# Optimization experiments

Hardware: AMD Instinct MI355X
Metric: run time of the kernel (lower is better)

The kernel has to match this reference:

```python
import jax, jax.numpy as jnp
import numpy as np

GAMMA = 1.0
BIG = 1e10  # finite stand-in for +inf (keeps logsumexp/vjp NaN-free; exp(-BIG/gamma)==0)


def _softmin3(a, b, c, gamma):
    # -gamma * logsumexp(-x/gamma) over the three candidates
    s = jnp.stack([a, b, c], axis=0) * (-1.0 / gamma)
    return -gamma * jax.scipy.special.logsumexp(s, axis=0)


def _softdtw(D, gamma):
    """Soft-DTW cost via anti-diagonal wavefront scan.
    D: (B, N, M) distance matrix. Returns (B,) soft-DTW cost R[N, M].
    Diagonal d holds cells (i, j) with i + j == d; stored as length-(N+1)
    vectors indexed by i, invalid cells = BIG.
    """
    B, N, M = D.shape
    ii = jnp.arange(N)  # ii = i - 1 for cells i = 1..N on a diagonal

    # diagonal d=0: only R[0,0]=0; diagonal d=1: all padded-inf cells
    r_d0 = jnp.full((B, N + 1), BIG, D.dtype).at[:, 0].set(0.0)
    r_d1 = jnp.full((B, N + 1), BIG, D.dtype)

    def step(carry, d):
        rp2, rp1 = carry  # diagonals d-2 and d-1, each (B, N+1)
        jj = d - 2 - ii  # jj = j - 1 = d - i - 1 for each cell on diagonal d
        valid = (jj >= 0) & (jj < M)  # j in 1..M (i in 1..N by construction)
        d_vals = D[:, ii, jnp.clip(jj, 0, M - 1)]  # (B, N): D[:, i-1, j-1]
        # cell i uses R[i-1,j-1]=rp2[i-1], R[i-1,j]=rp1[i-1], R[i,j-1]=rp1[i]
        sm = _softmin3(rp2[:, :-1], rp1[:, :-1], rp1[:, 1:], gamma)  # (B, N)
        new_inner = jnp.where(valid[None, :], d_vals + sm, BIG)
        row0 = jnp.full((B, 1), BIG, D.dtype)  # i = 0 row is always inf for d >= 2
        new_diag = jnp.concatenate([row0, new_inner], axis=1)  # (B, N+1)
        return (rp1, new_diag), None

    (_, r_last), _ = jax.lax.scan(step, (r_d0, r_d1), jnp.arange(2, N + M + 1))
    return r_last[:, N]  # R[N, M]


def setup_inputs() -> dict:
    key = jax.random.key(0)
    D = jax.random.uniform(key, (64, 1024, 1024), dtype=jnp.float32)
    return {"D": D}


def reference(D):
    return _softdtw(D, GAMMA)
```

## Files before the change

### kernel.cpp

```cpp
#include <hip/hip_runtime.h>


#define LOG2E 1.4426950408889634f
#define LN2  0.6931471805599453f

constexpr int N = 1024;
constexpr int TPB = 64;
constexpr int KC = 8;
constexpr int RQ = 4;
constexpr int NQ = N / RQ;
constexpr int NPAN = 2;
constexpr int PC = N / NPAN;
constexpr int ITER = 320;
constexpr unsigned long long POISON = 0xFFFFFFFFFFFFFFFFull;

__device__ __forceinline__ float fexp2(float x){float r;asm("v_exp_f32 %0, %1":"=v"(r):"v"(x));return r;}
__device__ __forceinline__ float flog2(float x){float r;asm("v_log_f32 %0, %1":"=v"(r):"v"(x));return r;}
__device__ __forceinline__ int   ffrexpe(float x){int r;asm("v_frexp_exp_i32_f32 %0, %1":"=v"(r):"v"(x));return r;}
__device__ __forceinline__ float fldexp(float x, int e){float r;asm("v_ldexp_f32 %0, %1, %2":"=v"(r):"v"(x),"v"(e));return r;}

__device__ __forceinline__ unsigned long long packv(float a, float b){
    return ((unsigned long long)__float_as_uint(b) << 32) | __float_as_uint(a);
}
__device__ __forceinline__ unsigned long long ldrelax(const unsigned long long* p){
    return __hip_atomic_load(p, __ATOMIC_RELAXED, __HIP_MEMORY_SCOPE_AGENT);
}

__global__ __launch_bounds__(TPB, 1)
void softdtw_kernel(const float* __restrict__ D, float* __restrict__ out,
                    unsigned long long* __restrict__ pay){
    const int blk = blockIdx.x;
    const int b = blk & 63;
    const int q = blk >> 6;
    const int t = threadIdx.x;
    const float* __restrict__ bp = D + (size_t)b * N * N + q * PC + t * KC;

    const bool isProd = (t == TPB - 1) && (q == 0);
    const bool isCons = (t == 0) && (q == 1);
    const size_t base = (size_t)b * NQ * 2;

    float pW[KC] = {0,0,0,0,0,0,0,0};
    int   S = 0;
    float luW = (t == 0 && q == 0) ? 1.0f : 0.0f;
    float exW[RQ] = {0,0,0,0};
    int   exS = 0;
    float nW[RQ] = {0,0,0,0};
    int   nS = 0;

    unsigned long long rg[8][2];
#pragma unroll
    for (int i = 0; i < 8; ++i) { rg[i][0] = POISON; rg[i][1] = POISON; }
    if (isCons) {
#pragma unroll
        for (int i = 0; i < 8; ++i) {
            rg[i][0] = ldrelax(&pay[base + (size_t)i * 2 + 0]);
            rg[i][1] = ldrelax(&pay[base + (size_t)i * 2 + 1]);
        }
    }

    float4 ld[2][RQ][2];
#pragma unroll
    for (int x = 0; x < 2; ++x) {
        int pc = min(max(x - t, 0), NQ - 1);
        const float* a = bp + (size_t)(pc * RQ) * N;
#pragma unroll
        for (int r = 0; r < RQ; ++r) {
            ld[x][r][0] = *(const float4*)(a + (size_t)r * N);
            ld[x][r][1] = *(const float4*)(a + (size_t)r * N + 4);
        }
    }
    __builtin_amdgcn_sched_barrier(0);

    for (int jb = 0; jb < ITER; jb += 8) {
#pragma unroll
        for (int u = 0; u < 8; ++u) {
            const int p = jb + u - t;
            const bool active = (unsigned)p < (unsigned)NQ;
            const int slot = u & 1;

            float cv0 = 0, cv1 = 0, cv2 = 0, cv3 = 0;
            if (isCons && active) {
                unsigned long long w0 = rg[u][0];
                unsigned long long w1 = rg[u][1];
                while (w0 == POISON) w0 = ldrelax(&pay[base + (size_t)p * 2 + 0]);
                while (w1 == POISON) w1 = ldrelax(&pay[base + (size_t)p * 2 + 1]);
                cv0 = __uint_as_float((unsigned)(w0 & 0xFFFFFFFFu));
                cv1 = __uint_as_float((unsigned)(w0 >> 32));
                cv2 = __uint_as_float((unsigned)(w1 & 0xFFFFFFFFu));
                cv3 = __uint_as_float((unsigned)(w1 >> 32));
            }

            const int iS = nS;
            if (p == 0) {
                if (isCons) S = (int)(0.0f - cv0);
                else if (t == 0 && q == 0) S = 0;
                else S = iS;
            }

            float eW[RQ];
            {
                const int dS = iS - S;
                eW[0] = fldexp(nW[0], dS); eW[1] = fldexp(nW[1], dS);
                eW[2] = fldexp(nW[2], dS); eW[3] = fldexp(nW[3], dS);
            }
            if (t == 0 && q == 0) { eW[0] = eW[1] = eW[2] = eW[3] = 0.0f; }
            if (isCons) {
                const float Sf = (float)S;
                eW[0] = fexp2(0.0f - cv0 - Sf);
                eW[1] = fexp2(0.0f - cv1 - Sf);
                eW[2] = fexp2(0.0f - cv2 - Sf);
                eW[3] = fexp2(0.0f - cv3 - Sf);
            }

            float a0 = pW[0], a1 = pW[1], a2 = pW[2], a3 = pW[3];
            float a4 = pW[4], a5 = pW[5], a6 = pW[6], a7 = pW[7];
            float dg = luW;
            float eR[RQ];
#pragma unroll
            for (int r = 0; r < RQ; ++r) {
                const float4 d0 = ld[slot][r][0];
                const float4 d1 = ld[slot][r][1];
                float f0 = fexp2(-LOG2E * d0.x), f1 = fexp2(-LOG2E * d0.y);
                float f2 = fexp2(-LOG2E * d0.z), f3 = fexp2(-LOG2E * d0.w);
                float f4 = fexp2(-LOG2E * d1.x), f5 = fexp2(-LOG2E * d1.y);
                float f6 = fexp2(-LOG2E * d1.z), f7 = fexp2(-LOG2E * d1.w);
                float s01 = a0 + a1, s12 = a1 + a2, s23 = a2 + a3, s34 = a3 + a4;
                float s45 = a4 + a5, s56 = a5 + a6, s67 = a6 + a7;
                float t0 = dg + eW[r];
                float W0 = f0 * (a0 + t0);
                float W1 = f1 * (s01 + W0);
                float W2 = f2 * (s12 + W1);
                float W3 = f3 * (s23 + W2);
                float W4 = f4 * (s34 + W3);
                float W5 = f5 * (s45 + W4);
                float W6 = f6 * (s56 + W5);
                float W7 = f7 * (s67 + W6);
                eR[r] = W7;
                dg = eW[r];
                a0 = W0; a1 = W1; a2 = W2; a3 = W3;
                a4 = W4; a5 = W5; a6 = W6; a7 = W7;
            }

            const int e = ffrexpe(a7);
            const float sc = fldexp(1.0f, -e);

            if (active) {
                pW[0] = a0 * sc; pW[1] = a1 * sc; pW[2] = a2 * sc; pW[3] = a3 * sc;
                pW[4] = a4 * sc; pW[5] = a5 * sc; pW[6] = a6 * sc; pW[7] = a7 * sc;
                luW = dg * sc;
                exW[0] = eR[0] * sc; exW[1] = eR[1] * sc;
                exW[2] = eR[2] * sc; exW[3] = eR[3] * sc;
                S += e; exS = S;
            }

            if (isProd && active) {
                const float Sf = (float)S;
                float v0 = 0.0f - (flog2(exW[0]) + Sf);
                float v1 = 0.0f - (flog2(exW[1]) + Sf);
                float v2 = 0.0f - (flog2(exW[2]) + Sf);
                float v3 = 0.0f - (flog2(exW[3]) + Sf);
                __hip_atomic_store(&pay[base + (size_t)p * 2 + 0], packv(v0, v1), __ATOMIC_RELAXED, __HIP_MEMORY_SCOPE_AGENT);
                __hip_atomic_store(&pay[base + (size_t)p * 2 + 1], packv(v2, v3), __ATOMIC_RELAXED, __HIP_MEMORY_SCOPE_AGENT);
            }

            {
                int pc = min(max(p + 2, 0), NQ - 1);
                const float* a = bp + (size_t)(pc * RQ) * N;
#pragma unroll
                for (int r = 0; r < RQ; ++r) {
                    ld[slot][r][0] = *(const float4*)(a + (size_t)r * N);
                    ld[slot][r][1] = *(const float4*)(a + (size_t)r * N + 4);
                }
            }
            __builtin_amdgcn_sched_barrier(0);

            if (isCons && (p + 8) < NQ) {
                rg[u][0] = ldrelax(&pay[base + (size_t)(p + 8) * 2 + 0]);
                rg[u][1] = ldrelax(&pay[base + (size_t)(p + 8) * 2 + 1]);
            }

            nW[0] = __shfl_up(exW[0], 1);
            nW[1] = __shfl_up(exW[1], 1);
            nW[2] = __shfl_up(exW[2], 1);
            nW[3] = __shfl_up(exW[3], 1);
            nS    = __shfl_up(exS, 1);
        }
    }

    if (q == NPAN - 1 && t == TPB - 1)
        out[b] = -(flog2(pW[KC - 1]) + (float)S) * LN2;
}

extern "C" void kernel_launch(void* const* d_in, const int* in_sizes, int n_in,
                              void* d_out, int out_size, void* d_ws, size_t ws_size,
                              hipStream_t stream) {
    const float* D = (const float*)d_in[0];
    float* out = (float*)d_out;
    const int B = in_sizes[0] / (N * N);

    unsigned long long* pay = (unsigned long long*)d_ws;
    const size_t payBytes = (size_t)B * NQ * 2 * sizeof(unsigned long long);

    hipMemsetAsync(d_ws, 0xFF, payBytes, stream);

    softdtw_kernel<<<B * NPAN, TPB, 0, stream>>>(D, out, pay);
}
```

Measured before the change: 254.6 us.

## Add producer wavefront that stages D tiles in LDS for compute wave

```diff
diff --git a/kernel.cpp b/kernel.cpp
--- a/kernel.cpp
+++ b/kernel.cpp
@@ -5,7 +5,7 @@
 #define LN2  0.6931471805599453f
 
 constexpr int N = 1024;
-constexpr int TPB = 64;
+constexpr int TPB = 128;
 constexpr int KC = 8;
 constexpr int RQ = 4;
 constexpr int NQ = N / RQ;
@@ -18,7 +18,9 @@
 __device__ __forceinline__ float flog2(float x){float r;asm("v_log_f32 %0, %1":"=v"(r):"v"(x));return r;}
 __device__ __forceinline__ int   ffrexpe(float x){int r;asm("v_frexp_exp_i32_f32 %0, %1":"=v"(r):"v"(x));return r;}
 __device__ __forceinline__ float fldexp(float x, int e){float r;asm("v_ldexp_f32 %0, %1, %2":"=v"(r):"v"(x),"v"(e));return r;}
-
+__device__ __forceinline__ void gload4(float4& d, const float* p){
+    asm volatile("global_load_dwordx4 %0, %1, off" : "=v"(d) : "v"(p));
+}
 __device__ __forceinline__ unsigned long long packv(float a, float b){
     return ((unsigned long long)__float_as_uint(b) << 32) | __float_as_uint(a);
 }
@@ -33,15 +35,69 @@
     const int b = blk & 63;
     const int q = blk >> 6;
     const int t = threadIdx.x;
-    const float* __restrict__ bp = D + (size_t)b * N * N + q * PC + t * KC;
-
-    const bool isProd = (t == TPB - 1) && (q == 0);
-    const bool isCons = (t == 0) && (q == 1);
+    const int lg = t & 63;
+    const int w = t >> 6;
+    const float* __restrict__ bp = D + (size_t)b * N * N + q * PC + lg * KC;
     const size_t base = (size_t)b * NQ * 2;
+
+    __shared__ float4 tile[4][RQ][2][64];
+    __shared__ int lseqv;
+    __shared__ int cdonev;
+    if (t == 0) { lseqv = -1; cdonev = -1; }
+    __syncthreads();
+
+    if (w == 1) {
+        float4 A[RQ][2], B[RQ][2];
+        const float* a0;
+        {
+            int pc = min(max(0 - lg, 0), NQ - 1);
+            a0 = bp + (size_t)(pc * RQ) * N;
+#pragma unroll
+            for (int r = 0; r < RQ; ++r) { gload4(A[r][0], a0 + (size_t)r * N); gload4(A[r][1], a0 + (size_t)r * N + 4); }
+            pc = min(max(1 - lg, 0), NQ - 1);
+            a0 = bp + (size_t)(pc * RQ) * N;
+#pragma unroll
+            for (int r = 0; r < RQ; ++r) { gload4(B[r][0], a0 + (size_t)r * N); gload4(B[r][1], a0 + (size_t)r * N + 4); }
+        }
+        for (int jb = 0; jb < ITER; jb += 2) {
+            {
+                const int jt = jb;
+                if (jt >= 4) { while (*(volatile int*)&cdonev < jt - 4) {} }
+                asm volatile("s_waitcnt vmcnt(8)" ::: "memory");
+                __builtin_amdgcn_sched_barrier(0);
+#pragma unroll
+                for (int r = 0; r < RQ; ++r) { tile[jt & 3][r][0][lg] = A[r][0]; tile[jt & 3][r][1][lg] = A[r][1]; }
+                asm volatile("s_waitcnt lgkmcnt(0)" ::: "memory");
+                *(volatile int*)&lseqv = jt;
+                int pc = min(max(jt + 2 - lg, 0), NQ - 1);
+                const float* a = bp + (size_t)(pc * RQ) * N;
+#pragma unroll
+                for (int r = 0; r < RQ; ++r) { gload4(A[r][0], a + (size_t)r * N); gload4(A[r][1], a + (size_t)r * N + 4); }
+            }
+            {
+                const int jt = jb + 1;
+                if (jt >= 4) { while (*(volatile int*)&cdonev < jt - 4) {} }
+                asm volatile("s_waitcnt vmcnt(8)" ::: "memory");
+                __builtin_amdgcn_sched_barrier(0);
+#pragma unroll
+                for (int r = 0; r < RQ; ++r) { tile[jt & 3][r][0][lg] = B[r][0]; tile[jt & 3][r][1][lg] = B[r][1]; }
+                asm volatile("s_waitcnt lgkmcnt(0)" ::: "memory");
+                *(volatile int*)&lseqv = jt;
+                int pc = min(max(jt + 2 - lg, 0), NQ - 1);
+                const float* a = bp + (size_t)(pc * RQ) * N;
+#pragma unroll
+                for (int r = 0; r < RQ; ++r) { gload4(B[r][0], a + (size_t)r * N); gload4(B[r][1], a + (size_t)r * N + 4); }
+            }
+        }
+        return;
+    }
+
+    const bool isProd = (lg == 63) && (q == 0);
+    const bool isCons = (lg == 0) && (q == 1);
 
     float pW[KC] = {0,0,0,0,0,0,0,0};
     int   S = 0;
-    float luW = (t == 0 && q == 0) ? 1.0f : 0.0f;
+    float luW = (lg == 0 && q == 0) ? 1.0f : 0.0f;
     float exW[RQ] = {0,0,0,0};
     int   exS = 0;
     float nW[RQ] = {0,0,0,0};
@@ -58,25 +114,12 @@
         }
     }
 
-    float4 ld[2][RQ][2];
-#pragma unroll
-    for (int x = 0; x < 2; ++x) {
-        int pc = min(max(x - t, 0), NQ - 1);
-        const float* a = bp + (size_t)(pc * RQ) * N;
-#pragma unroll
-        for (int r = 0; r < RQ; ++r) {
-            ld[x][r][0] = *(const float4*)(a + (size_t)r * N);
-            ld[x][r][1] = *(const float4*)(a + (size_t)r * N + 4);
-        }
-    }
-    __builtin_amdgcn_sched_barrier(0);
-
     for (int jb = 0; jb < ITER; jb += 8) {
 #pragma unroll
         for (int u = 0; u < 8; ++u) {
-            const int p = jb + u - t;
+            const int j = jb + u;
+            const int p = j - lg;
             const bool active = (unsigned)p < (unsigned)NQ;
-            const int slot = u & 1;
 
             float cv0 = 0, cv1 = 0, cv2 = 0, cv3 = 0;
             if (isCons && active) {
@@ -93,7 +136,7 @@
             const int iS = nS;
             if (p == 0) {
                 if (isCons) S = (int)(0.0f - cv0);
-                else if (t == 0 && q == 0) S = 0;
+                else if (lg == 0 && q == 0) S = 0;
                 else S = iS;
             }
 
@@ -103,7 +146,7 @@
                 eW[0] = fldexp(nW[0], dS); eW[1] = fldexp(nW[1], dS);
                 eW[2] = fldexp(nW[2], dS); eW[3] = fldexp(nW[3], dS);
             }
-            if (t == 0 && q == 0) { eW[0] = eW[1] = eW[2] = eW[3] = 0.0f; }
+            if (lg == 0 && q == 0) { eW[0] = eW[1] = eW[2] = eW[3] = 0.0f; }
             if (isCons) {
                 const float Sf = (float)S;
                 eW[0] = fexp2(0.0f - cv0 - Sf);
@@ -112,14 +155,20 @@
                 eW[3] = fexp2(0.0f - cv3 - Sf);
             }
 
+            while (*(volatile int*)&lseqv < j) {}
+            asm volatile("" ::: "memory");
+            float4 d0r[RQ], d1r[RQ];
+#pragma unroll
+            for (int r = 0; r < RQ; ++r) { d0r[r] = tile[j & 3][r][0][lg]; d1r[r] = tile[j & 3][r][1][lg]; }
+
             float a0 = pW[0], a1 = pW[1], a2 = pW[2], a3 = pW[3];
             float a4 = pW[4], a5 = pW[5], a6 = pW[6], a7 = pW[7];
             float dg = luW;
             float eR[RQ];
 #pragma unroll
             for (int r = 0; r < RQ; ++r) {
-                const float4 d0 = ld[slot][r][0];
-                const float4 d1 = ld[slot][r][1];
+                const float4 d0 = d0r[r];
+                const float4 d1 = d1r[r];
                 float f0 = fexp2(-LOG2E * d0.x), f1 = fexp2(-LOG2E * d0.y);
                 float f2 = fexp2(-LOG2E * d0.z), f3 = fexp2(-LOG2E * d0.w);
                 float f4 = fexp2(-LOG2E * d1.x), f5 = fexp2(-LOG2E * d1.y);
@@ -163,16 +212,8 @@
                 __hip_atomic_store(&pay[base + (size_t)p * 2 + 1], packv(v2, v3), __ATOMIC_RELAXED, __HIP_MEMORY_SCOPE_AGENT);
             }
 
-            {
-                int pc = min(max(p + 2, 0), NQ - 1);
-                const float* a = bp + (size_t)(pc * RQ) * N;
-#pragma unroll
-                for (int r = 0; r < RQ; ++r) {
-                    ld[slot][r][0] = *(const float4*)(a + (size_t)r * N);
-                    ld[slot][r][1] = *(const float4*)(a + (size_t)r * N + 4);
-                }
-            }
-            __builtin_amdgcn_sched_barrier(0);
+            asm volatile("" ::: "memory");
+            if (lg == 0) *(volatile int*)&cdonev = j;
 
             if (isCons && (p + 8) < NQ) {
                 rg[u][0] = ldrelax(&pay[base + (size_t)(p + 8) * 2 + 0]);
@@ -187,7 +228,7 @@
         }
     }
 
-    if (q == NPAN - 1 && t == TPB - 1)
+    if (q == NPAN - 1 && lg == 63)
         out[b] = -(flog2(pW[KC - 1]) + (float)S) * LN2;
 }
 
```

New measurement: 341.0 us. +34.0%, slower.

## Precompute exp(-D) into a per-thread contiguous strip layout in a prepass

Applied to the files above, without the earlier changes.

```diff
diff --git a/kernel.cpp b/kernel.cpp
--- a/kernel.cpp
+++ b/kernel.cpp
@@ -14,11 +14,15 @@
 constexpr int ITER = 320;
 constexpr unsigned long long POISON = 0xFFFFFFFFFFFFFFFFull;
 
+constexpr int STRIP_FLOATS = NQ * 32;
+constexpr int JOB_FLOATS   = 64 * STRIP_FLOATS;
+constexpr size_t MBOX_BYTES = (size_t)64 * NQ * 2 * sizeof(unsigned long long);
+constexpr size_t DP_BYTES   = (size_t)128 * JOB_FLOATS * sizeof(float);
+
 __device__ __forceinline__ float fexp2(float x){float r;asm("v_exp_f32 %0, %1":"=v"(r):"v"(x));return r;}
 __device__ __forceinline__ float flog2(float x){float r;asm("v_log_f32 %0, %1":"=v"(r):"v"(x));return r;}
 __device__ __forceinline__ int   ffrexpe(float x){int r;asm("v_frexp_exp_i32_f32 %0, %1":"=v"(r):"v"(x));return r;}
 __device__ __forceinline__ float fldexp(float x, int e){float r;asm("v_ldexp_f32 %0, %1, %2":"=v"(r):"v"(x),"v"(e));return r;}
-
 __device__ __forceinline__ unsigned long long packv(float a, float b){
     return ((unsigned long long)__float_as_uint(b) << 32) | __float_as_uint(a);
 }
@@ -26,14 +30,68 @@
     return __hip_atomic_load(p, __ATOMIC_RELAXED, __HIP_MEMORY_SCOPE_AGENT);
 }
 
+__global__ __launch_bounds__(256)
+void prepass_kernel(const float* __restrict__ D, float* __restrict__ Dp){
+    const int blk = blockIdx.x;
+    const int rb  = blk & 7;
+    const int g   = (blk >> 3) & 15;
+    const int job = blk >> 7;
+    const int b = job & 63, q = job >> 6;
+    const int tid = threadIdx.x;
+
+    __shared__ float lds[128 * 33];
+
+    {
+        const int row  = tid >> 1;
+        const int half = tid & 1;
+        const float* src = D + (size_t)b * N * N + (size_t)(rb * 128 + row) * N
+                         + q * PC + g * 32 + half * 16;
+        float4 v0 = *(const float4*)(src + 0);
+        float4 v1 = *(const float4*)(src + 4);
+        float4 v2 = *(const float4*)(src + 8);
+        float4 v3 = *(const float4*)(src + 12);
+        float* l = &lds[row * 33 + half * 16];
+        l[0]  = fexp2(-LOG2E * v0.x); l[1]  = fexp2(-LOG2E * v0.y);
+        l[2]  = fexp2(-LOG2E * v0.z); l[3]  = fexp2(-LOG2E * v0.w);
+        l[4]  = fexp2(-LOG2E * v1.x); l[5]  = fexp2(-LOG2E * v1.y);
+        l[6]  = fexp2(-LOG2E * v1.z); l[7]  = fexp2(-LOG2E * v1.w);
+        l[8]  = fexp2(-LOG2E * v2.x); l[9]  = fexp2(-LOG2E * v2.y);
+        l[10] = fexp2(-LOG2E * v2.z); l[11] = fexp2(-LOG2E * v2.w);
+        l[12] = fexp2(-LOG2E * v3.x); l[13] = fexp2(-LOG2E * v3.y);
+        l[14] = fexp2(-LOG2E * v3.z); l[15] = fexp2(-LOG2E * v3.w);
+    }
+    __syncthreads();
+
+    {
+        const int u    = tid >> 1;
+        const int half = tid & 1;
+        const int s    = u >> 5;
+        const int pl   = u & 31;
+        float o[16];
+#pragma unroll
+        for (int r2 = 0; r2 < 2; ++r2)
+#pragma unroll
+            for (int k = 0; k < 8; ++k)
+                o[r2 * 8 + k] = lds[(4 * pl + 2 * half + r2) * 33 + s * 8 + k];
+        float* dst = Dp + (size_t)job * JOB_FLOATS
+                   + (size_t)(g * 4 + s) * STRIP_FLOATS
+                   + (size_t)(rb * 32 + pl) * 32 + half * 16;
+        *(float4*)(dst + 0)  = make_float4(o[0], o[1], o[2], o[3]);
+        *(float4*)(dst + 4)  = make_float4(o[4], o[5], o[6], o[7]);
+        *(float4*)(dst + 8)  = make_float4(o[8], o[9], o[10], o[11]);
+        *(float4*)(dst + 12) = make_float4(o[12], o[13], o[14], o[15]);
+    }
+}
+
 __global__ __launch_bounds__(TPB, 1)
-void softdtw_kernel(const float* __restrict__ D, float* __restrict__ out,
+void softdtw_kernel(const float* __restrict__ Dp, float* __restrict__ out,
                     unsigned long long* __restrict__ pay){
     const int blk = blockIdx.x;
     const int b = blk & 63;
     const int q = blk >> 6;
     const int t = threadIdx.x;
-    const float* __restrict__ bp = D + (size_t)b * N * N + q * PC + t * KC;
+    const float* __restrict__ sp = Dp + (size_t)(q * 64 + b) * JOB_FLOATS
+                                 + (size_t)t * STRIP_FLOATS;
 
     const bool isProd = (t == TPB - 1) && (q == 0);
     const bool isCons = (t == 0) && (q == 1);
@@ -58,16 +116,13 @@
         }
     }
 
-    float4 ld[2][RQ][2];
+    float4 ld[2][8];
 #pragma unroll
     for (int x = 0; x < 2; ++x) {
         int pc = min(max(x - t, 0), NQ - 1);
-        const float* a = bp + (size_t)(pc * RQ) * N;
-#pragma unroll
-        for (int r = 0; r < RQ; ++r) {
-            ld[x][r][0] = *(const float4*)(a + (size_t)r * N);
-            ld[x][r][1] = *(const float4*)(a + (size_t)r * N + 4);
-        }
+        const float* a = sp + (size_t)pc * 32;
+#pragma unroll
+        for (int h = 0; h < 8; ++h) ld[x][h] = *(const float4*)(a + 4 * h);
     }
     __builtin_amdgcn_sched_barrier(0);
 
@@ -118,23 +173,19 @@
             float eR[RQ];
 #pragma unroll
             for (int r = 0; r < RQ; ++r) {
-                const float4 d0 = ld[slot][r][0];
-                const float4 d1 = ld[slot][r][1];
-                float f0 = fexp2(-LOG2E * d0.x), f1 = fexp2(-LOG2E * d0.y);
-                float f2 = fexp2(-LOG2E * d0.z), f3 = fexp2(-LOG2E * d0.w);
-                float f4 = fexp2(-LOG2E * d1.x), f5 = fexp2(-LOG2E * d1.y);
-                float f6 = fexp2(-LOG2E * d1.z), f7 = fexp2(-LOG2E * d1.w);
+                const float4 fa = ld[slot][r * 2 + 0];
+                const float4 fb = ld[slot][r * 2 + 1];
                 float s01 = a0 + a1, s12 = a1 + a2, s23 = a2 + a3, s34 = a3 + a4;
                 float s45 = a4 + a5, s56 = a5 + a6, s67 = a6 + a7;
                 float t0 = dg + eW[r];
-                float W0 = f0 * (a0 + t0);
-                float W1 = f1 * (s01 + W0);
-                float W2 = f2 * (s12 + W1);
-                float W3 = f3 * (s23 + W2);
-                float W4 = f4 * (s34 + W3);
-                float W5 = f5 * (s45 + W4);
-                float W6 = f6 * (s56 + W5);
-                float W7 = f7 * (s67 + W6);
+                float W0 = fa.x * (a0 + t0);
+                float W1 = fa.y * (s01 + W0);
+                float W2 = fa.z * (s12 + W1);
+                float W3 = fa.w * (s23 + W2);
+                float W4 = fb.x * (s34 + W3);
+                float W5 = fb.y * (s45 + W4);
+                float W6 = fb.z * (s56 + W5);
+                float W7 = fb.w * (s67 + W6);
                 eR[r] = W7;
                 dg = eW[r];
                 a0 = W0; a1 = W1; a2 = W2; a3 = W3;
@@ -165,12 +216,9 @@
 
             {
                 int pc = min(max(p + 2, 0), NQ - 1);
-                const float* a = bp + (size_t)(pc * RQ) * N;
-#pragma unroll
-                for (int r = 0; r < RQ; ++r) {
-                    ld[slot][r][0] = *(const float4*)(a + (size_t)r * N);
-                    ld[slot][r][1] = *(const float4*)(a + (size_t)r * N + 4);
-                }
+                const float* a = sp + (size_t)pc * 32;
+#pragma unroll
+                for (int h = 0; h < 8; ++h) ld[slot][h] = *(const float4*)(a + 4 * h);
             }
             __builtin_amdgcn_sched_barrier(0);
 
@@ -191,6 +239,120 @@
         out[b] = -(flog2(pW[KC - 1]) + (float)S) * LN2;
 }
 
+__global__ __launch_bounds__(TPB, 1)
+void softdtw_fb(const float* __restrict__ D, float* __restrict__ out,
+                unsigned long long* __restrict__ pay){
+    const int blk = blockIdx.x;
+    const int b = blk & 63, q = blk >> 6;
+    const int t = threadIdx.x;
+    const float* __restrict__ bp = D + (size_t)b * N * N + q * PC + t * KC;
+    const bool isProd = (t == TPB - 1) && (q == 0);
+    const bool isCons = (t == 0) && (q == 1);
+    const size_t base = (size_t)b * NQ * 2;
+    float pW[KC] = {0,0,0,0,0,0,0,0};
+    int S = 0; float luW = (t == 0 && q == 0) ? 1.0f : 0.0f;
+    float exW[RQ] = {0,0,0,0}; int exS = 0;
+    float nW[RQ] = {0,0,0,0}; int nS = 0;
+    unsigned long long rg[8][2];
+#pragma unroll
+    for (int i = 0; i < 8; ++i) { rg[i][0] = POISON; rg[i][1] = POISON; }
+    if (isCons) {
+#pragma unroll
+        for (int i = 0; i < 8; ++i) {
+            rg[i][0] = ldrelax(&pay[base + (size_t)i * 2 + 0]);
+            rg[i][1] = ldrelax(&pay[base + (size_t)i * 2 + 1]);
+        }
+    }
+    float4 ld[2][RQ][2];
+#pragma unroll
+    for (int x = 0; x < 2; ++x) {
+        int pc = min(max(x - t, 0), NQ - 1);
+        const float* a = bp + (size_t)(pc * RQ) * N;
+#pragma unroll
+        for (int r = 0; r < RQ; ++r) { ld[x][r][0] = *(const float4*)(a + (size_t)r * N); ld[x][r][1] = *(const float4*)(a + (size_t)r * N + 4); }
+    }
+    __builtin_amdgcn_sched_barrier(0);
+    for (int jb = 0; jb < ITER; jb += 8) {
+#pragma unroll
+        for (int u = 0; u < 8; ++u) {
+            const int p = jb + u - t;
+            const bool active = (unsigned)p < (unsigned)NQ;
+            const int slot = u & 1;
+            float cv0 = 0, cv1 = 0, cv2 = 0, cv3 = 0;
+            if (isCons && active) {
+                unsigned long long w0 = rg[u][0], w1 = rg[u][1];
+                while (w0 == POISON) w0 = ldrelax(&pay[base + (size_t)p * 2 + 0]);
+                while (w1 == POISON) w1 = ldrelax(&pay[base + (size_t)p * 2 + 1]);
+                cv0 = __uint_as_float((unsigned)(w0 & 0xFFFFFFFFu));
+                cv1 = __uint_as_float((unsigned)(w0 >> 32));
+                cv2 = __uint_as_float((unsigned)(w1 & 0xFFFFFFFFu));
+                cv3 = __uint_as_float((unsigned)(w1 >> 32));
+            }
+            const int iS = nS;
+            if (p == 0) { if (isCons) S = (int)(0.0f - cv0); else if (t == 0 && q == 0) S = 0; else S = iS; }
+            float eW[RQ];
+            { const int dS = iS - S;
+              eW[0] = fldexp(nW[0], dS); eW[1] = fldexp(nW[1], dS);
+              eW[2] = fldexp(nW[2], dS); eW[3] = fldexp(nW[3], dS); }
+            if (t == 0 && q == 0) { eW[0] = eW[1] = eW[2] = eW[3] = 0.0f; }
+            if (isCons) {
+                const float Sf = (float)S;
+                eW[0] = fexp2(0.0f - cv0 - Sf); eW[1] = fexp2(0.0f - cv1 - Sf);
+                eW[2] = fexp2(0.0f - cv2 - Sf); eW[3] = fexp2(0.0f - cv3 - Sf);
+            }
+            float a0 = pW[0], a1 = pW[1], a2 = pW[2], a3 = pW[3];
+            float a4 = pW[4], a5 = pW[5], a6 = pW[6], a7 = pW[7];
+            float dg = luW; float eR[RQ];
+#pragma unroll
+            for (int r = 0; r < RQ; ++r) {
+                const float4 d0 = ld[slot][r][0]; const float4 d1 = ld[slot][r][1];
+                float f0 = fexp2(-LOG2E * d0.x), f1 = fexp2(-LOG2E * d0.y);
+                float f2 = fexp2(-LOG2E * d0.z), f3 = fexp2(-LOG2E * d0.w);
+                float f4 = fexp2(-LOG2E * d1.x), f5 = fexp2(-LOG2E * d1.y);
+                float f6 = fexp2(-LOG2E * d1.z), f7 = fexp2(-LOG2E * d1.w);
+                float s01 = a0 + a1, s12 = a1 + a2, s23 = a2 + a3, s34 = a3 + a4;
+                float s45 = a4 + a5, s56 = a5 + a6, s67 = a6 + a7;
+                float t0 = dg + eW[r];
+                float W0 = f0 * (a0 + t0); float W1 = f1 * (s01 + W0);
+                float W2 = f2 * (s12 + W1); float W3 = f3 * (s23 + W2);
+                float W4 = f4 * (s34 + W3); float W5 = f5 * (s45 + W4);
+                float W6 = f6 * (s56 + W5); float W7 = f7 * (s67 + W6);
+                eR[r] = W7; dg = eW[r];
+                a0 = W0; a1 = W1; a2 = W2; a3 = W3; a4 = W4; a5 = W5; a6 = W6; a7 = W7;
+            }
+            const int e = ffrexpe(a7); const float sc = fldexp(1.0f, -e);
+            if (active) {
+                pW[0] = a0 * sc; pW[1] = a1 * sc; pW[2] = a2 * sc; pW[3] = a3 * sc;
+                pW[4] = a4 * sc; pW[5] = a5 * sc; pW[6] = a6 * sc; pW[7] = a7 * sc;
+                luW = dg * sc;
+                exW[0] = eR[0] * sc; exW[1] = eR[1] * sc; exW[2] = eR[2] * sc; exW[3] = eR[3] * sc;
+                S += e; exS = S;
+            }
+            if (isProd && active) {
+                const float Sf = (float)S;
+                float v0 = 0.0f - (flog2(exW[0]) + Sf), v1 = 0.0f - (flog2(exW[1]) + Sf);
+                float v2 = 0.0f - (flog2(exW[2]) + Sf), v3 = 0.0f - (flog2(exW[3]) + Sf);
+                __hip_atomic_store(&pay[base + (size_t)p * 2 + 0], packv(v0, v1), __ATOMIC_RELAXED, __HIP_MEMORY_SCOPE_AGENT);
+                __hip_atomic_store(&pay[base + (size_t)p * 2 + 1], packv(v2, v3), __ATOMIC_RELAXED, __HIP_MEMORY_SCOPE_AGENT);
+            }
+            { int pc = min(max(p + 2, 0), NQ - 1);
+              const float* a = bp + (size_t)(pc * RQ) * N;
+#pragma unroll
+              for (int r = 0; r < RQ; ++r) { ld[slot][r][0] = *(const float4*)(a + (size_t)r * N); ld[slot][r][1] = *(const float4*)(a + (size_t)r * N + 4); } }
+            __builtin_amdgcn_sched_barrier(0);
+            if (isCons && (p + 8) < NQ) {
+                rg[u][0] = ldrelax(&pay[base + (size_t)(p + 8) * 2 + 0]);
+                rg[u][1] = ldrelax(&pay[base + (size_t)(p + 8) * 2 + 1]);
+            }
+            nW[0] = __shfl_up(exW[0], 1); nW[1] = __shfl_up(exW[1], 1);
+            nW[2] = __shfl_up(exW[2], 1); nW[3] = __shfl_up(exW[3], 1);
+            nS = __shfl_up(exS, 1);
+        }
+    }
+    if (q == NPAN - 1 && t == TPB - 1)
+        out[b] = -(flog2(pW[KC - 1]) + (float)S) * LN2;
+}
+
 extern "C" void kernel_launch(void* const* d_in, const int* in_sizes, int n_in,
                               void* d_out, int out_size, void* d_ws, size_t ws_size,
                               hipStream_t stream) {
@@ -199,9 +361,13 @@
     const int B = in_sizes[0] / (N * N);
 
     unsigned long long* pay = (unsigned long long*)d_ws;
-    const size_t payBytes = (size_t)B * NQ * 2 * sizeof(unsigned long long);
-
-    hipMemsetAsync(d_ws, 0xFF, payBytes, stream);
-
-    softdtw_kernel<<<B * NPAN, TPB, 0, stream>>>(D, out, pay);
-}
+    hipMemsetAsync(d_ws, 0xFF, MBOX_BYTES, stream);
+
+    if (ws_size >= MBOX_BYTES + DP_BYTES && B == 64) {
+        float* Dp = (float*)((char*)d_ws + MBOX_BYTES);
+        prepass_kernel<<<128 * 16 * 8, 256, 0, stream>>>(D, Dp);
+        softdtw_kernel<<<B * NPAN, TPB, 0, stream>>>(Dp, out, pay);
+    } else {
+        softdtw_fb<<<B * NPAN, TPB, 0, stream>>>(D, out, pay);
+    }
+}
```

Result: slower. 370.7 us (+45.6%).
